# Performance work log

Hardware: AMD Instinct MI355X
Metric: run time of the kernel (lower is better)

## Reference

```python
import jax, jax.numpy as jnp
import numpy as np

D_MODEL = 2048
HEADS = 16
K = D_MODEL // HEADS  # 128
FFN = 8192


def rms_norm(x):
    # mean of squares over last dim, no eps (matches source)
    ms = jnp.mean(jnp.square(x), axis=2, keepdims=True)
    return x / jnp.sqrt(ms)


def setup_inputs() -> dict:
    key = jax.random.key(0)
    ks = jax.random.split(key, 9)
    s = D_MODEL ** (-0.5)
    B, S = 2, 2048
    return {
        "x_BSE": jax.random.normal(ks[0], (B, S, D_MODEL), jnp.float32),
        "w_q": jax.random.normal(ks[1], (D_MODEL, HEADS, K), jnp.float32) * s,
        "w_k": jax.random.normal(ks[2], (D_MODEL, HEADS, K), jnp.float32) * s,
        "w_v": jax.random.normal(ks[3], (D_MODEL, HEADS, K), jnp.float32) * s,
        "w_o": jax.random.normal(ks[4], (D_MODEL, HEADS, K), jnp.float32) * s,
        "w1": jax.random.normal(ks[5], (D_MODEL, FFN), jnp.float32) * s,
        "b1": jax.random.normal(ks[6], (1, FFN), jnp.float32) * s,
        "w2": jax.random.normal(ks[7], (FFN, D_MODEL), jnp.float32) * s,
        "b2": jax.random.normal(ks[8], (1, D_MODEL), jnp.float32) * s,
    }


def attention(x, w_q, w_k, w_v, w_o):
    q = jnp.einsum('bse,ehk->bshk', x, w_q)
    k = jnp.einsum('bme,ehk->bmhk', x, w_k)
    v = jnp.einsum('bme,ehk->bmhk', x, w_v)
    logits = jnp.einsum('bshk,bmhk->bshm', q, k) / jnp.sqrt(jnp.float32(K))
    S = x.shape[1]
    causal = jnp.arange(S)[:, None] >= jnp.arange(S)[None, :]  # [S, M]
    logits = jnp.where(causal[None, :, None, :], logits, -jnp.inf)
    probs = jax.nn.softmax(logits, axis=3)
    out = jnp.einsum('bshm,bmhk->bshk', probs, v)
    return jnp.einsum('bshk,ehk->bse', out, w_o)


def ffn(x, w1, b1, w2, b2):
    h = jnp.clip(x @ w1 + b1, 0.0, 6.0)  # ReLU6
    return h @ w2 + b2


def reference(x_BSE, w_q, w_k, w_v, w_o, w1, b1, w2, b2):
    x = x_BSE + attention(rms_norm(x_BSE), w_q, w_k, w_v, w_o)
    x = x + ffn(rms_norm(x), w1, b1, w2, b2)
    return x
```

## Files before the change

### kernel.cpp

```cpp
#include <hip/hip_runtime.h>
#include <hip/hip_bf16.h>
#include <stdint.h>

typedef __attribute__((ext_vector_type(8))) short bf16x8;
typedef __attribute__((ext_vector_type(4))) float f32x4;

typedef __attribute__((address_space(1))) char as1_char;
typedef __attribute__((address_space(3))) char as3_char;

__device__ __forceinline__ void gload_lds16(const void* g, void* l) {
  __builtin_amdgcn_global_load_lds((as1_char*)g, (as3_char*)l, 16, 0, 0);
}

__device__ __forceinline__ unsigned short f2bf(float f) {
  union { float f; unsigned u; } c; c.f = f;
  unsigned u = c.u;
  return (unsigned short)((u + 0x7fffu + ((u >> 16) & 1u)) >> 16);
}

__global__ __launch_bounds__(256)
void rmsnorm_kernel(const float* __restrict__ x, unsigned short* __restrict__ out) {
  const int tok = blockIdx.x;
  const int tid = threadIdx.x;
  const float4* xr = (const float4*)(x + (size_t)tok * 2048);
  float4 a = xr[tid];
  float4 b = xr[tid + 256];
  float s = a.x*a.x + a.y*a.y + a.z*a.z + a.w*a.w
          + b.x*b.x + b.y*b.y + b.z*b.z + b.w*b.w;
  #pragma unroll
  for (int m = 1; m < 64; m <<= 1) s += __shfl_xor(s, m);
  __shared__ float ws4[4];
  if ((tid & 63) == 0) ws4[tid >> 6] = s;
  __syncthreads();
  const float tot = ws4[0] + ws4[1] + ws4[2] + ws4[3];
  const float r = rsqrtf(tot * (1.0f / 2048.0f));
  ushort4 o1, o2;
  o1.x = f2bf(a.x * r); o1.y = f2bf(a.y * r); o1.z = f2bf(a.z * r); o1.w = f2bf(a.w * r);
  o2.x = f2bf(b.x * r); o2.y = f2bf(b.y * r); o2.z = f2bf(b.z * r); o2.w = f2bf(b.w * r);
  ushort4* orow = (ushort4*)(out + (size_t)tok * 2048);
  orow[tid] = o1;
  orow[tid + 256] = o2;
}

__global__ __launch_bounds__(256)
void transpose_cvt(const float* __restrict__ in, unsigned short* __restrict__ out,
                   int R, int C) {
  __shared__ float t[32][33];
  const int c0 = blockIdx.x * 32, r0 = blockIdx.y * 32;
  const int tx = threadIdx.x, ty = threadIdx.y;
  #pragma unroll
  for (int i = 0; i < 4; i++)
    t[ty + 8 * i][tx] = in[(size_t)(r0 + ty + 8 * i) * C + (c0 + tx)];
  __syncthreads();
  #pragma unroll
  for (int i = 0; i < 4; i++)
    out[(size_t)(c0 + ty + 8 * i) * R + (r0 + tx)] = f2bf(t[tx][ty + 8 * i]);
}

__global__ __launch_bounds__(256)
void cvt_bf16_kernel(const float* __restrict__ in, unsigned short* __restrict__ out, int n4) {
  const int i = blockIdx.x * 256 + threadIdx.x;
  if (i < n4) {
    float4 v = ((const float4*)in)[i];
    ushort4 o; o.x = f2bf(v.x); o.y = f2bf(v.y); o.z = f2bf(v.z); o.w = f2bf(v.w);
    ((ushort4*)out)[i] = o;
  }
}

template <int EPI>
__global__ __launch_bounds__(256)
void gemm_bt(const unsigned short* __restrict__ A,
             const unsigned short* __restrict__ B,
             int K, int N,
             unsigned short* outb, float* outf,
             const float* res, const float* bias) {
  __shared__ __align__(16) unsigned short As[128 * 64];
  __shared__ __align__(16) unsigned short Bs[128 * 64];
  const int tid = threadIdx.x;
  const int lane = tid & 63;
  const int wid = tid >> 6;
  const int wm = wid >> 1, wn = wid & 1;
  const int ln15 = lane & 15, g = lane >> 4;
  const int m0 = blockIdx.y * 128, n0 = blockIdx.x * 128;

  f32x4 acc[4][4] = {};
  const char* Abase = (const char*)(A + (size_t)m0 * K);
  const char* Bbase = (const char*)(B + (size_t)n0 * K);
  const size_t rowb = (size_t)K * 2;

  for (int k0 = 0; k0 < K; k0 += 64) {
    __syncthreads();
    #pragma unroll
    for (int i = 0; i < 4; i++) {
      const int o = i * 4096 + tid * 16;
      const int row = o >> 7;
      const int scb = (o & 127) ^ ((row & 7) << 4);
      gload_lds16(Abase + (size_t)row * rowb + (size_t)k0 * 2 + scb, (char*)As + o);
      gload_lds16(Bbase + (size_t)row * rowb + (size_t)k0 * 2 + scb, (char*)Bs + o);
    }
    __syncthreads();
    #pragma unroll
    for (int kk = 0; kk < 2; kk++) {
      bf16x8 af[4], bfr[4];
      #pragma unroll
      for (int mi = 0; mi < 4; mi++) {
        const int row = wm * 64 + mi * 16 + ln15;
        const int cb = kk * 64 + g * 16;
        af[mi] = *(const bf16x8*)((const char*)As + row * 128 + (cb ^ ((row & 7) << 4)));
      }
      #pragma unroll
      for (int ni = 0; ni < 4; ni++) {
        const int row = wn * 64 + ni * 16 + ln15;
        const int cb = kk * 64 + g * 16;
        bfr[ni] = *(const bf16x8*)((const char*)Bs + row * 128 + (cb ^ ((row & 7) << 4)));
      }
      #pragma unroll
      for (int mi = 0; mi < 4; mi++)
        #pragma unroll
        for (int ni = 0; ni < 4; ni++)
          acc[mi][ni] = __builtin_amdgcn_mfma_f32_16x16x32_bf16(af[mi], bfr[ni], acc[mi][ni], 0, 0, 0);
    }
  }

  #pragma unroll
  for (int mi = 0; mi < 4; mi++) {
    const int mrow = m0 + wm * 64 + mi * 16 + g * 4;
    #pragma unroll
    for (int ni = 0; ni < 4; ni++) {
      const int ncol = n0 + wn * 64 + ni * 16 + ln15;
      if (EPI == 0) {
        #pragma unroll
        for (int r = 0; r < 4; r++)
          outb[(size_t)(mrow + r) * N + ncol] = f2bf(acc[mi][ni][r]);
      } else if (EPI == 1) {
        const int bb = mrow >> 11, ss = mrow & 2047;
        const int hh = ncol >> 7, dd = ncol & 127;
        ushort4 v;
        v.x = f2bf(acc[mi][ni][0]); v.y = f2bf(acc[mi][ni][1]);
        v.z = f2bf(acc[mi][ni][2]); v.w = f2bf(acc[mi][ni][3]);
        *(ushort4*)(outb + ((size_t)((bb * 16 + hh) * 128 + dd)) * 2048 + ss) = v;
      } else if (EPI == 2) {
        const float bv = bias[ncol];
        #pragma unroll
        for (int r = 0; r < 4; r++) {
          float v = acc[mi][ni][r] + bv;
          v = fminf(fmaxf(v, 0.0f), 6.0f);
          outb[(size_t)(mrow + r) * N + ncol] = f2bf(v);
        }
      } else {
        const float bv = bias ? bias[ncol] : 0.0f;
        #pragma unroll
        for (int r = 0; r < 4; r++) {
          const size_t idx = (size_t)(mrow + r) * N + ncol;
          outf[idx] = res[idx] + acc[mi][ni][r] + bv;
        }
      }
    }
  }
}

__global__ __launch_bounds__(256)
void attn_kernel(const unsigned short* __restrict__ Qg,
                 const unsigned short* __restrict__ Kg,
                 const unsigned short* __restrict__ Vg,
                 unsigned short* __restrict__ Og) {
  __shared__ __align__(16) char smem[65536];
  const int tid = threadIdx.x, lane = tid & 63, wid = tid >> 6;
  const int g = lane >> 4, qq = lane & 15;
  const int pairx = blockIdx.x, h = blockIdx.y, b = blockIdx.z;

  auto stage = [&](int kv0, char* kdst, char* vdst) {
    #pragma unroll
    for (int i = 0; i < 4; i++) {
      const int oo = i * 4096 + tid * 16;
      const int rK = oo >> 8;
      const int sK = (oo & 255) ^ ((rK & 7) << 4);
      gload_lds16((const char*)Kg + ((size_t)(b * 2048 + kv0 + rK) * 2048 + h * 128) * 2 + sK,
                  kdst + oo);
      const int rV = oo >> 7;
      const int sV = (oo & 127) ^ ((rV & 7) << 4);
      gload_lds16((const char*)Vg + ((size_t)((b * 16 + h) * 128 + rV) * 2048 + kv0) * 2 + sV,
                  vdst + oo);
    }
  };

  for (int half = 0; half < 2; ++half) {
    const int qb = half ? (31 - pairx) : pairx;
    const int q0 = qb * 64;
    const int myq = q0 + wid * 16 + qq;
    const int nt = qb + 1;

    bf16x8 qf[4];
    const unsigned short* qp = Qg + ((size_t)(b * 2048 + myq)) * 2048 + h * 128 + g * 8;
    #pragma unroll
    for (int ks = 0; ks < 4; ks++) qf[ks] = *(const bf16x8*)(qp + ks * 32);

    stage(0, smem, smem + 16384);

    float m_run = -1e30f, l_run = 0.0f;
    f32x4 oacc[8] = {};

    for (int t = 0; t < nt; ++t) {
      const int cur = t & 1;
      char* kbc = cur ? smem + 32768 : smem;
      char* vbc = cur ? smem + 49152 : smem + 16384;
      char* kbn = cur ? smem : smem + 32768;
      char* vbn = cur ? smem + 16384 : smem + 49152;

      if (t + 1 < nt) {
        stage((t + 1) * 64, kbn, vbn);
        asm volatile("s_waitcnt vmcnt(8)" ::: "memory");
      } else {
        asm volatile("s_waitcnt vmcnt(0)" ::: "memory");
      }
      __builtin_amdgcn_s_barrier();
      asm volatile("" ::: "memory");

      const int kv0 = t * 64;

      f32x4 st[4] = {};
      __builtin_amdgcn_s_setprio(1);
      #pragma unroll
      for (int ks = 0; ks < 4; ks++) {
        #pragma unroll
        for (int f = 0; f < 4; f++) {
          const int row = f * 16 + qq;
          const int cb = ks * 64 + g * 16;
          bf16x8 kf = *(const bf16x8*)(kbc + row * 256 + (cb ^ ((row & 7) << 4)));
          st[f] = __builtin_amdgcn_mfma_f32_16x16x32_bf16(kf, qf[ks], st[f], 0, 0, 0);
        }
      }
      __builtin_amdgcn_s_setprio(0);

      float p[4][4];
      float tmax = -3.0e38f;
      const bool diag = (t == qb);
      #pragma unroll
      for (int f = 0; f < 4; f++) {
        #pragma unroll
        for (int r = 0; r < 4; r++) {
          float v = st[f][r] * 0.08838834764831845f;
          if (diag) {
            const int kv = kv0 + f * 16 + g * 4 + r;
            if (kv > myq) v = -3.0e38f;
          }
          p[f][r] = v;
          tmax = fmaxf(tmax, v);
        }
      }
      tmax = fmaxf(tmax, __shfl_xor(tmax, 16));
      tmax = fmaxf(tmax, __shfl_xor(tmax, 32));
      const float m_new = fmaxf(m_run, tmax);
      const float sf = __expf(m_run - m_new);
      m_run = m_new;
      float tsum = 0.0f;
      #pragma unroll
      for (int f = 0; f < 4; f++) {
        #pragma unroll
        for (int r = 0; r < 4; r++) {
          p[f][r] = __expf(p[f][r] - m_new);
          tsum += p[f][r];
        }
      }
      tsum += __shfl_xor(tsum, 16);
      tsum += __shfl_xor(tsum, 32);
      l_run = l_run * sf + tsum;

      unsigned pk[4][2];
      #pragma unroll
      for (int f = 0; f < 4; f++) {
        pk[f][0] = (unsigned)f2bf(p[f][0]) | ((unsigned)f2bf(p[f][1]) << 16);
        pk[f][1] = (unsigned)f2bf(p[f][2]) | ((unsigned)f2bf(p[f][3]) << 16);
      }
      bf16x8 pa[2];
      const int sel = g >> 1;
      #pragma unroll
      for (int ks2 = 0; ks2 < 2; ks2++) {
        unsigned d[4];
        #pragma unroll
        for (int u = 0; u < 2; u++) {
          const int sl = qq + (((2 * g + u) & 3) << 4);
          const unsigned lo0 = (unsigned)__shfl((int)pk[2 * ks2][0], sl);
          const unsigned hi0 = (unsigned)__shfl((int)pk[2 * ks2 + 1][0], sl);
          const unsigned lo1 = (unsigned)__shfl((int)pk[2 * ks2][1], sl);
          const unsigned hi1 = (unsigned)__shfl((int)pk[2 * ks2 + 1][1], sl);
          d[2 * u]     = sel ? hi0 : lo0;
          d[2 * u + 1] = sel ? hi1 : lo1;
        }
        union { unsigned u[4]; bf16x8 v; } cv;
        cv.u[0] = d[0]; cv.u[1] = d[1]; cv.u[2] = d[2]; cv.u[3] = d[3];
        pa[ks2] = cv.v;
      }

      float sfr[4];
      #pragma unroll
      for (int r = 0; r < 4; r++) sfr[r] = __shfl(sf, g * 4 + r);
      #pragma unroll
      for (int nf = 0; nf < 8; nf++) {
        oacc[nf][0] *= sfr[0]; oacc[nf][1] *= sfr[1];
        oacc[nf][2] *= sfr[2]; oacc[nf][3] *= sfr[3];
      }
      __builtin_amdgcn_s_setprio(1);
      #pragma unroll
      for (int nf = 0; nf < 8; nf++) {
        #pragma unroll
        for (int ks2 = 0; ks2 < 2; ks2++) {
          const int row = nf * 16 + qq;
          const int cb = ks2 * 64 + g * 16;
          bf16x8 vf = *(const bf16x8*)(vbc + row * 128 + (cb ^ ((row & 7) << 4)));
          oacc[nf] = __builtin_amdgcn_mfma_f32_16x16x32_bf16(pa[ks2], vf, oacc[nf], 0, 0, 0);
        }
      }
      __builtin_amdgcn_s_setprio(0);

      asm volatile("" ::: "memory");
      __builtin_amdgcn_s_barrier();
    }

    asm volatile("" ::: "memory");
    const float inv = 1.0f / l_run;
    float invr[4];
    #pragma unroll
    for (int r = 0; r < 4; r++) invr[r] = __shfl(inv, g * 4 + r);

    float* Osm = (float*)smem;
    #pragma unroll
    for (int nf = 0; nf < 8; nf++) {
      #pragma unroll
      for (int r = 0; r < 4; r++)
        Osm[(wid * 16 + g * 4 + r) * 132 + nf * 16 + qq] = oacc[nf][r] * invr[r];
    }
    __syncthreads();
    #pragma unroll
    for (int it = 0; it < 4; it++) {
      const int row = it * 16 + (tid >> 4);
      const int c0 = (tid & 15) * 8;
      const float* src = &Osm[row * 132 + c0];
      uint4 w;
      w.x = (unsigned)f2bf(src[0]) | ((unsigned)f2bf(src[1]) << 16);
      w.y = (unsigned)f2bf(src[2]) | ((unsigned)f2bf(src[3]) << 16);
      w.z = (unsigned)f2bf(src[4]) | ((unsigned)f2bf(src[5]) << 16);
      w.w = (unsigned)f2bf(src[6]) | ((unsigned)f2bf(src[7]) << 16);
      *(uint4*)(Og + (size_t)(b * 2048 + q0 + row) * 2048 + h * 128 + c0) = w;
    }
    __syncthreads();
  }
}

extern "C" void kernel_launch(void* const* d_in, const int* in_sizes, int n_in,
                              void* d_out, int out_size, void* d_ws, size_t ws_size,
                              hipStream_t stream) {
  (void)in_sizes; (void)n_in; (void)out_size; (void)ws_size;
  const float* x  = (const float*)d_in[0];
  const float* wq = (const float*)d_in[1];
  const float* wk = (const float*)d_in[2];
  const float* wv = (const float*)d_in[3];
  const float* wo = (const float*)d_in[4];
  const float* w1 = (const float*)d_in[5];
  const float* b1 = (const float*)d_in[6];
  const float* w2 = (const float*)d_in[7];
  const float* b2 = (const float*)d_in[8];
  float* out = (float*)d_out;
  char* ws = (char*)d_ws;

  unsigned short* wqT = (unsigned short*)(ws + 0);
  unsigned short* wkT = (unsigned short*)(ws + 8388608);
  unsigned short* wvT = (unsigned short*)(ws + 16777216);
  unsigned short* woC = (unsigned short*)(ws + 25165824);
  unsigned short* w1T = (unsigned short*)(ws + 33554432);
  unsigned short* w2T = (unsigned short*)(ws + 67108864);
  unsigned short* h1  = (unsigned short*)(ws + 100663296);
  unsigned short* Qb  = (unsigned short*)(ws + 117440512);
  unsigned short* Kb  = (unsigned short*)(ws + 134217728);
  unsigned short* Vt  = (unsigned short*)(ws + 150994944);
  unsigned short* hid = h1;
  unsigned short* att = (unsigned short*)(ws + 167772160);
  unsigned short* h2  = att;

  const dim3 tb(32, 8);
  transpose_cvt<<<dim3(64, 64), tb, 0, stream>>>(wq, wqT, 2048, 2048);
  transpose_cvt<<<dim3(64, 64), tb, 0, stream>>>(wk, wkT, 2048, 2048);
  transpose_cvt<<<dim3(64, 64), tb, 0, stream>>>(wv, wvT, 2048, 2048);
  cvt_bf16_kernel<<<4096, 256, 0, stream>>>(wo, woC, 1048576);
  transpose_cvt<<<dim3(256, 64), tb, 0, stream>>>(w1, w1T, 2048, 8192);
  transpose_cvt<<<dim3(64, 256), tb, 0, stream>>>(w2, w2T, 8192, 2048);

  rmsnorm_kernel<<<4096, 256, 0, stream>>>(x, h1);
  gemm_bt<0><<<dim3(16, 32), 256, 0, stream>>>(h1, wqT, 2048, 2048, Qb, nullptr, nullptr, nullptr);
  gemm_bt<0><<<dim3(16, 32), 256, 0, stream>>>(h1, wkT, 2048, 2048, Kb, nullptr, nullptr, nullptr);
  gemm_bt<1><<<dim3(16, 32), 256, 0, stream>>>(h1, wvT, 2048, 2048, Vt, nullptr, nullptr, nullptr);
  attn_kernel<<<dim3(16, 16, 2), 256, 0, stream>>>(Qb, Kb, Vt, att);
  gemm_bt<3><<<dim3(16, 32), 256, 0, stream>>>(att, woC, 2048, 2048, nullptr, out, x, nullptr);
  rmsnorm_kernel<<<4096, 256, 0, stream>>>(out, h2);
  gemm_bt<2><<<dim3(64, 32), 256, 0, stream>>>(h2, w1T, 2048, 8192, hid, nullptr, nullptr, b1);
  gemm_bt<3><<<dim3(16, 32), 256, 0, stream>>>(hid, w2T, 8192, 2048, nullptr, out, out, b2);
}
```

Measured before the change: 726.7 us.

## Replace GEMM with 256-row multi-stage pipelined kernel and fuse QKV projections

After: 666.2 us. -8.3%, faster.

```diff
diff --git a/kernel.cpp b/kernel.cpp
--- a/kernel.cpp
+++ b/kernel.cpp
@@ -4,12 +4,17 @@
 
 typedef __attribute__((ext_vector_type(8))) short bf16x8;
 typedef __attribute__((ext_vector_type(4))) float f32x4;
+typedef unsigned short ushort_t;
 
 typedef __attribute__((address_space(1))) char as1_char;
 typedef __attribute__((address_space(3))) char as3_char;
 
 __device__ __forceinline__ void gload_lds16(const void* g, void* l) {
   __builtin_amdgcn_global_load_lds((as1_char*)g, (as3_char*)l, 16, 0, 0);
+}
+
+template <int N> __device__ __forceinline__ void waitvm() {
+  asm volatile("s_waitcnt vmcnt(%0)" :: "n"(N) : "memory");
 }
 
 __device__ __forceinline__ unsigned short f2bf(float f) {
@@ -67,85 +72,129 @@
   }
 }
 
-template <int EPI>
-__global__ __launch_bounds__(256)
-void gemm_bt(const unsigned short* __restrict__ A,
-             const unsigned short* __restrict__ B,
+template <int BN, int EPI>
+__global__ __launch_bounds__(512, 2)
+void gemm256(const ushort_t* __restrict__ A, const ushort_t* __restrict__ B,
              int K, int N,
-             unsigned short* outb, float* outf,
-             const float* res, const float* bias) {
-  __shared__ __align__(16) unsigned short As[128 * 64];
-  __shared__ __align__(16) unsigned short Bs[128 * 64];
+             ushort_t* ob0, ushort_t* ob1, ushort_t* ob2, float* outf,
+             const float* __restrict__ res, const float* __restrict__ bias,
+             int nbx) {
+  constexpr int LB = (BN * 64) / 8192;
+  constexpr int LPT = 2 + LB;
+  constexpr int NR = BN / 64;
+  constexpr int WN = BN / 4;
+  constexpr int BUFSZ = 16384 + BN * 64;
+  __shared__ __align__(16) char smem[4 * BUFSZ];
+
   const int tid = threadIdx.x;
   const int lane = tid & 63;
   const int wid = tid >> 6;
-  const int wm = wid >> 1, wn = wid & 1;
+  const int wm = wid >> 2, wn = wid & 3;
   const int ln15 = lane & 15, g = lane >> 4;
-  const int m0 = blockIdx.y * 128, n0 = blockIdx.x * 128;
-
-  f32x4 acc[4][4] = {};
-  const char* Abase = (const char*)(A + (size_t)m0 * K);
-  const char* Bbase = (const char*)(B + (size_t)n0 * K);
+
+  int wg = blockIdx.x;
+  const int cpx = gridDim.x >> 3;
+  wg = (wg & 7) * cpx + (wg >> 3);
+  const int bx = wg % nbx, by = wg / nbx;
+  const int m0 = by * 256, n0 = bx * BN;
+
+  const char* Ab = (const char*)(A + (size_t)m0 * K);
+  const char* Bb = (const char*)(B + (size_t)n0 * K);
   const size_t rowb = (size_t)K * 2;
-
-  for (int k0 = 0; k0 < K; k0 += 64) {
-    __syncthreads();
-    #pragma unroll
-    for (int i = 0; i < 4; i++) {
-      const int o = i * 4096 + tid * 16;
-      const int row = o >> 7;
-      const int scb = (o & 127) ^ ((row & 7) << 4);
-      gload_lds16(Abase + (size_t)row * rowb + (size_t)k0 * 2 + scb, (char*)As + o);
-      gload_lds16(Bbase + (size_t)row * rowb + (size_t)k0 * 2 + scb, (char*)Bs + o);
-    }
-    __syncthreads();
-    #pragma unroll
-    for (int kk = 0; kk < 2; kk++) {
-      bf16x8 af[4], bfr[4];
-      #pragma unroll
-      for (int mi = 0; mi < 4; mi++) {
-        const int row = wm * 64 + mi * 16 + ln15;
-        const int cb = kk * 64 + g * 16;
-        af[mi] = *(const bf16x8*)((const char*)As + row * 128 + (cb ^ ((row & 7) << 4)));
-      }
-      #pragma unroll
-      for (int ni = 0; ni < 4; ni++) {
-        const int row = wn * 64 + ni * 16 + ln15;
-        const int cb = kk * 64 + g * 16;
-        bfr[ni] = *(const bf16x8*)((const char*)Bs + row * 128 + (cb ^ ((row & 7) << 4)));
-      }
-      #pragma unroll
-      for (int mi = 0; mi < 4; mi++)
-        #pragma unroll
-        for (int ni = 0; ni < 4; ni++)
-          acc[mi][ni] = __builtin_amdgcn_mfma_f32_16x16x32_bf16(af[mi], bfr[ni], acc[mi][ni], 0, 0, 0);
-    }
+  const int NT = K >> 5;
+
+  auto stage = [&](int t, int s) {
+    char* As = smem + s * BUFSZ;
+    char* Bs = As + 16384;
+    const size_t kb = (size_t)t * 64;
+    #pragma unroll
+    for (int i = 0; i < 2; i++) {
+      const int o = i * 8192 + tid * 16;
+      const int row = o >> 6, col = o & 63;
+      gload_lds16(Ab + (size_t)row * rowb + kb + (col ^ ((row & 3) << 4)), As + o);
+    }
+    #pragma unroll
+    for (int i = 0; i < LB; i++) {
+      const int o = i * 8192 + tid * 16;
+      const int row = o >> 6, col = o & 63;
+      gload_lds16(Bb + (size_t)row * rowb + kb + (col ^ ((row & 3) << 4)), Bs + o);
+    }
+  };
+
+  f32x4 acc[8][NR] = {};
+
+  stage(0, 0); stage(1, 1); stage(2, 2);
+
+  for (int t = 0; t < NT; ++t) {
+    if (t + 3 < NT) {
+      stage(t + 3, (t + 3) & 3);
+      waitvm<3 * LPT>();
+    } else {
+      const int rem = NT - 1 - t;
+      if (rem >= 2)      waitvm<2 * LPT>();
+      else if (rem == 1) waitvm<LPT>();
+      else               waitvm<0>();
+    }
+    __builtin_amdgcn_s_barrier();
+
+    const char* As = smem + (t & 3) * BUFSZ;
+    const char* Bs = As + 16384;
+
+    bf16x8 af[8], bfm[NR];
+    #pragma unroll
+    for (int mi = 0; mi < 8; mi++) {
+      const int row = wm * 128 + mi * 16 + ln15;
+      af[mi] = *(const bf16x8*)(As + row * 64 + ((g * 16) ^ ((row & 3) << 4)));
+    }
+    #pragma unroll
+    for (int ni = 0; ni < NR; ni++) {
+      const int row = wn * WN + ni * 16 + ln15;
+      bfm[ni] = *(const bf16x8*)(Bs + row * 64 + ((g * 16) ^ ((row & 3) << 4)));
+    }
+    asm volatile("" ::: "memory");
+    __builtin_amdgcn_s_barrier();
+
+    __builtin_amdgcn_s_setprio(1);
+    #pragma unroll
+    for (int mi = 0; mi < 8; mi++)
+      #pragma unroll
+      for (int ni = 0; ni < NR; ni++)
+        acc[mi][ni] = __builtin_amdgcn_mfma_f32_16x16x32_bf16(af[mi], bfm[ni], acc[mi][ni], 0, 0, 0);
+    __builtin_amdgcn_s_setprio(0);
   }
 
   #pragma unroll
-  for (int mi = 0; mi < 4; mi++) {
-    const int mrow = m0 + wm * 64 + mi * 16 + g * 4;
-    #pragma unroll
-    for (int ni = 0; ni < 4; ni++) {
-      const int ncol = n0 + wn * 64 + ni * 16 + ln15;
+  for (int mi = 0; mi < 8; mi++) {
+    const int mrow = m0 + wm * 128 + mi * 16 + g * 4;
+    #pragma unroll
+    for (int ni = 0; ni < NR; ni++) {
+      const int ncol = n0 + wn * WN + ni * 16 + ln15;
       if (EPI == 0) {
-        #pragma unroll
-        for (int r = 0; r < 4; r++)
-          outb[(size_t)(mrow + r) * N + ncol] = f2bf(acc[mi][ni][r]);
-      } else if (EPI == 1) {
-        const int bb = mrow >> 11, ss = mrow & 2047;
-        const int hh = ncol >> 7, dd = ncol & 127;
-        ushort4 v;
-        v.x = f2bf(acc[mi][ni][0]); v.y = f2bf(acc[mi][ni][1]);
-        v.z = f2bf(acc[mi][ni][2]); v.w = f2bf(acc[mi][ni][3]);
-        *(ushort4*)(outb + ((size_t)((bb * 16 + hh) * 128 + dd)) * 2048 + ss) = v;
+        const int region = n0 >> 11;
+        if (region == 0) {
+          #pragma unroll
+          for (int r = 0; r < 4; r++)
+            ob0[(size_t)(mrow + r) * 2048 + ncol] = f2bf(acc[mi][ni][r]);
+        } else if (region == 1) {
+          #pragma unroll
+          for (int r = 0; r < 4; r++)
+            ob1[(size_t)(mrow + r) * 2048 + (ncol - 2048)] = f2bf(acc[mi][ni][r]);
+        } else {
+          const int bb = mrow >> 11, ss = mrow & 2047;
+          const int ncv = ncol - 4096;
+          const int hh = ncv >> 7, dd = ncv & 127;
+          ushort4 v;
+          v.x = f2bf(acc[mi][ni][0]); v.y = f2bf(acc[mi][ni][1]);
+          v.z = f2bf(acc[mi][ni][2]); v.w = f2bf(acc[mi][ni][3]);
+          *(ushort4*)(ob2 + ((size_t)((bb * 16 + hh) * 128 + dd)) * 2048 + ss) = v;
+        }
       } else if (EPI == 2) {
         const float bv = bias[ncol];
         #pragma unroll
         for (int r = 0; r < 4; r++) {
           float v = acc[mi][ni][r] + bv;
           v = fminf(fmaxf(v, 0.0f), 6.0f);
-          outb[(size_t)(mrow + r) * N + ncol] = f2bf(v);
+          ob0[(size_t)(mrow + r) * N + ncol] = f2bf(v);
         }
       } else {
         const float bv = bias ? bias[ncol] : 0.0f;
@@ -363,19 +412,20 @@
   float* out = (float*)d_out;
   char* ws = (char*)d_ws;
 
-  unsigned short* wqT = (unsigned short*)(ws + 0);
-  unsigned short* wkT = (unsigned short*)(ws + 8388608);
-  unsigned short* wvT = (unsigned short*)(ws + 16777216);
-  unsigned short* woC = (unsigned short*)(ws + 25165824);
-  unsigned short* w1T = (unsigned short*)(ws + 33554432);
-  unsigned short* w2T = (unsigned short*)(ws + 67108864);
-  unsigned short* h1  = (unsigned short*)(ws + 100663296);
-  unsigned short* Qb  = (unsigned short*)(ws + 117440512);
-  unsigned short* Kb  = (unsigned short*)(ws + 134217728);
-  unsigned short* Vt  = (unsigned short*)(ws + 150994944);
-  unsigned short* hid = h1;
-  unsigned short* att = (unsigned short*)(ws + 167772160);
-  unsigned short* h2  = att;
+  ushort_t* wqkvT = (ushort_t*)(ws + 0);
+  ushort_t* wqT = wqkvT;
+  ushort_t* wkT = (ushort_t*)(ws + 8388608);
+  ushort_t* wvT = (ushort_t*)(ws + 16777216);
+  ushort_t* woC = (ushort_t*)(ws + 25165824);
+  ushort_t* w1T = (ushort_t*)(ws + 33554432);
+  ushort_t* w2T = (ushort_t*)(ws + 67108864);
+  ushort_t* h1  = (ushort_t*)(ws + 100663296);
+  ushort_t* Qb  = (ushort_t*)(ws + 117440512);
+  ushort_t* Kb  = (ushort_t*)(ws + 134217728);
+  ushort_t* Vt  = (ushort_t*)(ws + 150994944);
+  ushort_t* hid = h1;
+  ushort_t* att = (ushort_t*)(ws + 167772160);
+  ushort_t* h2  = att;
 
   const dim3 tb(32, 8);
   transpose_cvt<<<dim3(64, 64), tb, 0, stream>>>(wq, wqT, 2048, 2048);
@@ -386,12 +436,14 @@
   transpose_cvt<<<dim3(64, 256), tb, 0, stream>>>(w2, w2T, 8192, 2048);
 
   rmsnorm_kernel<<<4096, 256, 0, stream>>>(x, h1);
-  gemm_bt<0><<<dim3(16, 32), 256, 0, stream>>>(h1, wqT, 2048, 2048, Qb, nullptr, nullptr, nullptr);
-  gemm_bt<0><<<dim3(16, 32), 256, 0, stream>>>(h1, wkT, 2048, 2048, Kb, nullptr, nullptr, nullptr);
-  gemm_bt<1><<<dim3(16, 32), 256, 0, stream>>>(h1, wvT, 2048, 2048, Vt, nullptr, nullptr, nullptr);
+  gemm256<256, 0><<<24 * 16, 512, 0, stream>>>(h1, wqkvT, 2048, 6144,
+                                               Qb, Kb, Vt, nullptr, nullptr, nullptr, 24);
   attn_kernel<<<dim3(16, 16, 2), 256, 0, stream>>>(Qb, Kb, Vt, att);
-  gemm_bt<3><<<dim3(16, 32), 256, 0, stream>>>(att, woC, 2048, 2048, nullptr, out, x, nullptr);
+  gemm256<128, 3><<<16 * 16, 512, 0, stream>>>(att, woC, 2048, 2048,
+                                               nullptr, nullptr, nullptr, out, x, nullptr, 16);
   rmsnorm_kernel<<<4096, 256, 0, stream>>>(out, h2);
-  gemm_bt<2><<<dim3(64, 32), 256, 0, stream>>>(h2, w1T, 2048, 8192, hid, nullptr, nullptr, b1);
-  gemm_bt<3><<<dim3(16, 32), 256, 0, stream>>>(hid, w2T, 8192, 2048, nullptr, out, out, b2);
-}
+  gemm256<256, 2><<<32 * 16, 512, 0, stream>>>(h2, w1T, 2048, 8192,
+                                               hid, nullptr, nullptr, nullptr, nullptr, b1, 32);
+  gemm256<128, 3><<<16 * 16, 512, 0, stream>>>(hid, w2T, 8192, 2048,
+                                               nullptr, nullptr, nullptr, out, out, b2, 16);
+}
```
